# Performance work log

Hardware: AMD Instinct MI355X
Metric: run time of the kernel (lower is better)

## Reference

```python
import jax, jax.numpy as jnp
import numpy as np
import math

B, S, D, H = 2, 2048, 1024, 16
HD = D // H  # 64 head features


def setup_inputs() -> dict:
    key = jax.random.key(0)
    ks = jax.random.split(key, 6)
    x = jax.random.normal(ks[0], (B, S, D), jnp.float32)
    wq = jax.random.normal(ks[1], (D, D), jnp.float32) * 0.02
    wk = jax.random.normal(ks[2], (D, D), jnp.float32) * 0.02
    wv = jax.random.normal(ks[3], (D, D), jnp.float32) * 0.02
    wo = jax.random.normal(ks[4], (D, D), jnp.float32) * 0.02
    # Llama-style RoPE frequencies: unit-modulus complex per (pos, pair),
    # stored as separate cos/sin arrays of shape [S, HD//2].
    inv_freq = 1.0 / (10000.0 ** (jnp.arange(0, HD, 2, dtype=jnp.float32) / HD))
    ang = jnp.arange(S, dtype=jnp.float32)[:, None] * inv_freq[None, :]
    freq_cos = jnp.cos(ang)
    freq_sin = jnp.sin(ang)
    # realistic padding: each sequence keeps a random prefix of at least S//2 tokens
    lengths = jax.random.randint(ks[5], (B,), S // 2, S + 1)
    padding_mask = (jnp.arange(S)[None, :] < lengths[:, None]).astype(jnp.int32)
    return dict(x=x, wq=wq, wk=wk, wv=wv, wo=wo,
                freq_cos=freq_cos, freq_sin=freq_sin, padding_mask=padding_mask)


def _apply_rope(t, cos, sin):
    # t: [B, S, H, HD]; cos/sin: [S, HD//2]
    tr = t.reshape(t.shape[:-1] + (HD // 2, 2))
    t0, t1 = tr[..., 0], tr[..., 1]
    c = cos[None, :, None, :]
    s = sin[None, :, None, :]
    o0 = t0 * c - t1 * s  # real part of complex multiply
    o1 = t0 * s + t1 * c  # imag part
    return jnp.stack([o0, o1], axis=-1).reshape(t.shape)


def reference(x, wq, wk, wv, wo, freq_cos, freq_sin, padding_mask):
    # QKV projections (torch Linear: y = x @ W.T, no bias)
    q = (x @ wq.T).reshape(B, S, H, HD)
    k = (x @ wk.T).reshape(B, S, H, HD)
    v = (x @ wv.T).reshape(B, S, H, HD)
    q = _apply_rope(q, freq_cos, freq_sin)
    k = _apply_rope(k, freq_cos, freq_sin)
    q = jnp.transpose(q, (0, 2, 1, 3))  # [B,H,S,HD]
    k = jnp.transpose(k, (0, 2, 1, 3))
    v = jnp.transpose(v, (0, 2, 1, 3))
    # NOTE: original scales by sqrt(n_features), not sqrt(head_dim)
    scores = jnp.einsum('bhqd,bhkd->bhqk', q, k) / math.sqrt(D)
    bias = jnp.where(padding_mask[:, None, None, :] == 0,
                     jnp.float32(-jnp.inf), jnp.float32(0.0))
    p = jax.nn.softmax(scores + bias, axis=-1)
    out = jnp.einsum('bhqk,bhkd->bhqd', p, v)
    out = jnp.transpose(out, (0, 2, 1, 3)).reshape(B, S, D)
    return out @ wo.T
```

## Files before the change

### kernel.cpp

```cpp
#include <hip/hip_runtime.h>
#include <hip/hip_bf16.h>
#include <stdint.h>

typedef unsigned short u16;
typedef __attribute__((ext_vector_type(8))) short bf16x8;
typedef __attribute__((ext_vector_type(4))) float f32x4;
typedef __attribute__((ext_vector_type(16))) float f32x16;

__device__ __forceinline__ u16 f2bf(float f) {
  union { float f; uint32_t u; } a; a.f = f;
  return (u16)((a.u + 0x7FFFu + ((a.u >> 16) & 1u)) >> 16);
}

__device__ __forceinline__ void gload_lds16(const void* g, void* l) {
  auto* gp = (__attribute__((address_space(1))) void*)(uintptr_t)g;
  auto* lp = (__attribute__((address_space(3))) void*)(uintptr_t)l;
  __builtin_amdgcn_global_load_lds(gp, lp, 16, 0, 0);
}

__device__ __forceinline__ float exp2_fast(float x) {
  float r;
  asm("v_exp_f32 %0, %1" : "=v"(r) : "v"(x));
  return r;
}

#define CVTPK(d, a, b) asm("v_cvt_pk_bf16_f32 %0, %1, %2" : "=v"(d) : "v"(a), "v"(b))
#define SWAP32(a, b)   asm("v_permlane32_swap_b32 %0, %1" : "+v"(a), "+v"(b))
#define BARRIER() do { asm volatile("" ::: "memory"); __builtin_amdgcn_s_barrier(); asm volatile("" ::: "memory"); } while (0)
#define WAITVM0() asm volatile("s_waitcnt vmcnt(0)" ::: "memory")

__global__ void cvt_kernel(const float4* __restrict__ x, const float4* __restrict__ wq,
                           const float4* __restrict__ wk, const float4* __restrict__ wv,
                           const float4* __restrict__ wo,
                           ushort4* __restrict__ xb, ushort4* __restrict__ wqkv,
                           ushort4* __restrict__ wob) {
  const int XN = (2 * 2048 * 1024) / 4;
  const int WN = (1024 * 1024) / 4;
  const int total = XN + 4 * WN;
  for (int i = blockIdx.x * 256 + threadIdx.x; i < total; i += gridDim.x * 256) {
    float4 v; ushort4* dst;
    if (i < XN) { v = x[i]; dst = xb + i; }
    else {
      int j = i - XN; int m = j >> 18; int o = j & (WN - 1);
      const float4* src = (m == 0) ? wq : (m == 1) ? wk : (m == 2) ? wv : wo;
      v = src[o];
      dst = (m < 3) ? (wqkv + j) : (wob + o);
    }
    ushort4 r; r.x = f2bf(v.x); r.y = f2bf(v.y); r.z = f2bf(v.z); r.w = f2bf(v.w);
    *dst = r;
  }
}

__global__ void len_kernel(const int* __restrict__ mask, int* __restrict__ lens) {
  __shared__ int red[256];
  int b = blockIdx.x, s = 0;
  for (int i = threadIdx.x; i < 2048; i += 256) s += mask[b * 2048 + i];
  red[threadIdx.x] = s;
  __syncthreads();
  if (threadIdx.x < 64) {
    int v = red[threadIdx.x] + red[threadIdx.x + 64] + red[threadIdx.x + 128] + red[threadIdx.x + 192];
    #pragma unroll
    for (int o = 32; o > 0; o >>= 1) v += __shfl_down(v, o);
    if (threadIdx.x == 0) lens[b] = v;
  }
}

template <int BM, int BN, int MODE>
__global__ __launch_bounds__(256, 4)
void gemm2(const u16* __restrict__ A, const u16* __restrict__ Bm,
           int nTm, float* __restrict__ outf,
           u16* __restrict__ Qb, u16* __restrict__ Kb, u16* __restrict__ VbT,
           const float* __restrict__ cosT, const float* __restrict__ sinT) {
  constexpr int MREP = BM / 32;
  constexpr int NREP = BN / 32;
  constexpr int LA = BM / 64;
  constexpr int LB = BN / 64;
  __shared__ alignas(16) u16 SA[2][BM * 32];
  __shared__ alignas(16) u16 SB[2][BN * 32];

  const int tid = threadIdx.x, lane = tid & 63, wid = tid >> 6;
  const int wm = (wid >> 1) * (BM / 2), wn = (wid & 1) * (BN / 2);
  const int lr = lane & 15, lg = lane >> 4;

  const int cpx = gridDim.x >> 3;
  const int bid = (blockIdx.x & 7) * cpx + (blockIdx.x >> 3);
  const int m0 = (bid % nTm) * BM;
  const int n0 = (bid / nTm) * BN;

  const int srow = tid >> 2;
  const int schunk = (tid & 3) ^ (srow & 3);
  const u16* gA = A + (int64_t)(m0 + srow) * 1024 + schunk * 8;
  const u16* gB = Bm + (int64_t)(n0 + srow) * 1024 + schunk * 8;
  const int sdst = wid * 512;

#define STAGE(t) do { const int _b = (t) & 1, _ko = (t) * 32; \
    _Pragma("unroll") for (int j = 0; j < LA; ++j) \
      gload_lds16(gA + (int64_t)(j * 64) * 1024 + _ko, &SA[_b][j * 2048 + sdst]); \
    _Pragma("unroll") for (int j = 0; j < LB; ++j) \
      gload_lds16(gB + (int64_t)(j * 64) * 1024 + _ko, &SB[_b][j * 2048 + sdst]); } while (0)

  f32x4 acc[MREP][NREP];
  #pragma unroll
  for (int i = 0; i < MREP; ++i)
    #pragma unroll
    for (int j = 0; j < NREP; ++j)
      #pragma unroll
      for (int e = 0; e < 4; ++e) acc[i][j][e] = 0.0f;

  const int rchunk = (lg ^ (lr & 3)) * 8;

  STAGE(0);
  WAITVM0();
  BARRIER();

  for (int t = 0; t < 32; ++t) {
    if (t < 31) STAGE(t + 1);
    const u16* sa = SA[t & 1];
    const u16* sb = SB[t & 1];
    bf16x8 af[MREP], bfm[NREP];
    #pragma unroll
    for (int i = 0; i < MREP; ++i) af[i] = *(const bf16x8*)&sa[(wm + i * 16 + lr) * 32 + rchunk];
    #pragma unroll
    for (int i = 0; i < NREP; ++i) bfm[i] = *(const bf16x8*)&sb[(wn + i * 16 + lr) * 32 + rchunk];
    __builtin_amdgcn_s_setprio(1);
    #pragma unroll
    for (int mi = 0; mi < MREP; ++mi)
      #pragma unroll
      for (int ni = 0; ni < NREP; ++ni)
        acc[mi][ni] = __builtin_amdgcn_mfma_f32_16x16x32_bf16(af[mi], bfm[ni], acc[mi][ni], 0, 0, 0);
    __builtin_amdgcn_s_setprio(0);
    WAITVM0();
    BARRIER();
  }

  if (MODE == 0) {
    #pragma unroll
    for (int mi = 0; mi < MREP; ++mi)
      #pragma unroll
      for (int r = 0; r < 4; ++r) {
        const int row = m0 + wm + mi * 16 + lg * 4 + r;
        float* orow = outf + (int64_t)row * 1024 + n0 + wn + lr;
        #pragma unroll
        for (int ni = 0; ni < NREP; ++ni) orow[ni * 16] = acc[mi][ni][r];
      }
  } else {
    #pragma unroll
    for (int mi = 0; mi < MREP; ++mi) {
      #pragma unroll
      for (int r = 0; r < 4; ++r) {
        const int row = m0 + wm + mi * 16 + lg * 4 + r;
        const int bb = row >> 11, ss = row & 2047;
        #pragma unroll
        for (int ni = 0; ni < NREP; ++ni) {
          const int n = n0 + wn + ni * 16 + lr;
          float v = acc[mi][ni][r];
          if (n < 2048) {
            float partner = __shfl_xor(v, 1);
            const int ii = (n >> 1) & 31;
            const float c = cosT[ss * 32 + ii];
            const float sn = sinT[ss * 32 + ii];
            float rv = (n & 1) ? (partner * sn + v * c) : (v * c - partner * sn);
            const int h = (n >> 6) & 15, d = n & 63;
            const int idx = ((bb * 16 + h) * 2048 + ss) * 64 + d;
            if (n < 1024) Qb[idx] = f2bf(rv * 0.0450842298f);
            else          Kb[idx] = f2bf(rv);
          } else {
            const int n2 = n - 2048;
            const int h = n2 >> 6, d = n2 & 63;
            VbT[((int64_t)(bb * 16 + h) * 64 + d) * 2048 + ss] = f2bf(v);
          }
        }
      }
    }
  }
#undef STAGE
}

__global__ __launch_bounds__(256, 2)
void attn_kernel(const u16* __restrict__ Qb, const u16* __restrict__ Kb,
                 const u16* __restrict__ VbT, u16* __restrict__ attnb,
                 const int* __restrict__ lens) {
  __shared__ alignas(16) u16 Klds[2][64 * 64];
  __shared__ alignas(16) u16 Vlds[2][64 * 64];
  const int tid = threadIdx.x, lane = tid & 63, wid = tid >> 6;
  const int hi = lane >> 5, ql = lane & 31;
  const int bh = blockIdx.x >> 4;
  const int len = lens[bh >> 4];
  const int qrow = (blockIdx.x & 15) * 128 + wid * 32 + ql;

  bf16x8 qf[4];
  const u16* qptr = Qb + ((int64_t)bh * 2048 + qrow) * 64 + hi * 8;
  #pragma unroll
  for (int c = 0; c < 4; ++c) qf[c] = *(const bf16x8*)(qptr + c * 16);

  const int srow = tid >> 3, schunk = (tid & 7) ^ (srow & 7);
  const u16* kg = Kb + ((int64_t)bh * 2048 + srow) * 64 + schunk * 8;
  const u16* vg = VbT + ((int64_t)bh * 64 + srow) * 2048 + schunk * 8;
  const int dstoff = wid * 512;

  f32x16 oacc[2];
  #pragma unroll
  for (int r = 0; r < 16; ++r) { oacc[0][r] = 0.0f; oacc[1][r] = 0.0f; }
  float mrun = -1e30f, lrun = 0.0f;

  const int nt = (len + 63) >> 6;
  gload_lds16(kg,             &Klds[0][dstoff]);
  gload_lds16(kg + 32 * 64,   &Klds[0][2048 + dstoff]);
  gload_lds16(vg,             &Vlds[0][dstoff]);
  gload_lds16(vg + 32 * 2048, &Vlds[0][2048 + dstoff]);
  __syncthreads();

  const u16* kgn = kg + 64 * 64;
  const u16* vgn = vg + 64;

  for (int t = 0; t < nt; ++t) {
    const int bu = t & 1;
    if (t + 1 < nt) {
      gload_lds16(kgn,             &Klds[bu ^ 1][dstoff]);
      gload_lds16(kgn + 32 * 64,   &Klds[bu ^ 1][2048 + dstoff]);
      gload_lds16(vgn,             &Vlds[bu ^ 1][dstoff]);
      gload_lds16(vgn + 32 * 2048, &Vlds[bu ^ 1][2048 + dstoff]);
    }
    kgn += 64 * 64; vgn += 64;

    f32x16 s0, s1;
    #pragma unroll
    for (int r = 0; r < 16; ++r) { s0[r] = 0.0f; s1[r] = 0.0f; }
    __builtin_amdgcn_s_setprio(1);
    #pragma unroll
    for (int c = 0; c < 4; ++c) {
      const int slot = (((2 * c + hi) ^ (ql & 7)) * 8);
      bf16x8 kf0 = *(const bf16x8*)&Klds[bu][ql * 64 + slot];
      bf16x8 kf1 = *(const bf16x8*)&Klds[bu][(32 + ql) * 64 + slot];
      s0 = __builtin_amdgcn_mfma_f32_32x32x16_bf16(kf0, qf[c], s0, 0, 0, 0);
      s1 = __builtin_amdgcn_mfma_f32_32x32x16_bf16(kf1, qf[c], s1, 0, 0, 0);
    }
    __builtin_amdgcn_s_setprio(0);

    const int k0 = t * 64;
    if (k0 + 64 > len) {
      #pragma unroll
      for (int r = 0; r < 16; ++r) {
        const int key = k0 + (r & 3) + 8 * (r >> 2) + 4 * hi;
        if (key >= len) s0[r] = -1e30f;
        if (key + 32 >= len) s1[r] = -1e30f;
      }
    }

    float ma = fmaxf(s0[0], s1[0]), mb = fmaxf(s0[1], s1[1]);
    float mc = fmaxf(s0[2], s1[2]), md = fmaxf(s0[3], s1[3]);
    #pragma unroll
    for (int r = 4; r < 16; r += 4) {
      ma = fmaxf(ma, fmaxf(s0[r], s1[r]));
      mb = fmaxf(mb, fmaxf(s0[r + 1], s1[r + 1]));
      mc = fmaxf(mc, fmaxf(s0[r + 2], s1[r + 2]));
      md = fmaxf(md, fmaxf(s0[r + 3], s1[r + 3]));
    }
    float mx = fmaxf(fmaxf(ma, mb), fmaxf(mc, md));
    mx = fmaxf(mx, __shfl_xor(mx, 32));
    if (!__all(mx - mrun <= 11.0f)) {
      const float mnew = fmaxf(mrun, mx);
      const float sc = exp2_fast(mrun - mnew);
      #pragma unroll
      for (int r = 0; r < 16; ++r) { oacc[0][r] *= sc; oacc[1][r] *= sc; }
      lrun *= sc;
      mrun = mnew;
    }
    float p[32];
    float ps0 = 0.0f, ps1 = 0.0f, ps2 = 0.0f, ps3 = 0.0f;
    #pragma unroll
    for (int r = 0; r < 16; r += 4) {
      p[r]      = exp2_fast(s0[r] - mrun);
      p[r + 1]  = exp2_fast(s0[r + 1] - mrun);
      p[r + 2]  = exp2_fast(s0[r + 2] - mrun);
      p[r + 3]  = exp2_fast(s0[r + 3] - mrun);
      p[16 + r]     = exp2_fast(s1[r] - mrun);
      p[16 + r + 1] = exp2_fast(s1[r + 1] - mrun);
      p[16 + r + 2] = exp2_fast(s1[r + 2] - mrun);
      p[16 + r + 3] = exp2_fast(s1[r + 3] - mrun);
      ps0 += p[r] + p[16 + r];
      ps1 += p[r + 1] + p[16 + r + 1];
      ps2 += p[r + 2] + p[16 + r + 2];
      ps3 += p[r + 3] + p[16 + r + 3];
    }
    float psum = (ps0 + ps1) + (ps2 + ps3);
    psum += __shfl_xor(psum, 32);
    lrun += psum;

    bf16x8 pfrag[4];
    #pragma unroll
    for (int ks = 0; ks < 4; ++ks) {
      uint32_t a0, a1, a2, a3;
      CVTPK(a0, p[8 * ks + 0], p[8 * ks + 1]);
      CVTPK(a1, p[8 * ks + 2], p[8 * ks + 3]);
      CVTPK(a2, p[8 * ks + 4], p[8 * ks + 5]);
      CVTPK(a3, p[8 * ks + 6], p[8 * ks + 7]);
      SWAP32(a0, a2);
      SWAP32(a1, a3);
      union { uint32_t u[4]; bf16x8 v; } pw;
      pw.u[0] = a0; pw.u[1] = a1; pw.u[2] = a2; pw.u[3] = a3;
      pfrag[ks] = pw.v;
    }

    __builtin_amdgcn_s_setprio(1);
    #pragma unroll
    for (int dc = 0; dc < 2; ++dc) {
      const int drow = dc * 32 + ql;
      #pragma unroll
      for (int ks = 0; ks < 4; ++ks) {
        const int slot = (((2 * ks + hi) ^ (ql & 7)) * 8);
        bf16x8 vf = *(const bf16x8*)&Vlds[bu][drow * 64 + slot];
        oacc[dc] = __builtin_amdgcn_mfma_f32_32x32x16_bf16(vf, pfrag[ks], oacc[dc], 0, 0, 0);
      }
    }
    __builtin_amdgcn_s_setprio(0);
    __syncthreads();
  }

  const float inv = 1.0f / lrun;
  u16* outp = attnb + ((int64_t)((bh >> 4) * 2048 + qrow)) * 1024 + (bh & 15) * 64;
  #pragma unroll
  for (int dc = 0; dc < 2; ++dc)
    #pragma unroll
    for (int g = 0; g < 4; ++g) {
      ushort4 w;
      w.x = f2bf(oacc[dc][4 * g + 0] * inv);
      w.y = f2bf(oacc[dc][4 * g + 1] * inv);
      w.z = f2bf(oacc[dc][4 * g + 2] * inv);
      w.w = f2bf(oacc[dc][4 * g + 3] * inv);
      *(ushort4*)(outp + dc * 32 + 8 * g + 4 * hi) = w;
    }
}

extern "C" void kernel_launch(void* const* d_in, const int* in_sizes, int n_in,
                              void* d_out, int out_size, void* d_ws, size_t ws_size,
                              hipStream_t stream) {
  const float* x    = (const float*)d_in[0];
  const float* wq   = (const float*)d_in[1];
  const float* wk   = (const float*)d_in[2];
  const float* wv   = (const float*)d_in[3];
  const float* wo   = (const float*)d_in[4];
  const float* fcos = (const float*)d_in[5];
  const float* fsin = (const float*)d_in[6];
  const int*   pmsk = (const int*)d_in[7];
  float* out = (float*)d_out;

  char* ws = (char*)d_ws;
  u16* XB    = (u16*)(ws);
  u16* WQKV  = (u16*)(ws + (size_t)8  * 1048576);
  u16* WOB   = (u16*)(ws + (size_t)14 * 1048576);
  u16* QB    = (u16*)(ws + (size_t)16 * 1048576);
  u16* KB    = (u16*)(ws + (size_t)24 * 1048576);
  u16* VBT   = (u16*)(ws + (size_t)32 * 1048576);
  u16* ATTNB = (u16*)(ws + (size_t)40 * 1048576);
  int* LENS  = (int*)(ws + (size_t)48 * 1048576);

  cvt_kernel<<<2048, 256, 0, stream>>>((const float4*)x, (const float4*)wq,
                                       (const float4*)wk, (const float4*)wv,
                                       (const float4*)wo, (ushort4*)XB,
                                       (ushort4*)WQKV, (ushort4*)WOB);
  len_kernel<<<2, 256, 0, stream>>>(pmsk, LENS);

  gemm2<128, 128, 1><<<768, 256, 0, stream>>>(XB, WQKV, 32, nullptr,
                                              QB, KB, VBT, fcos, fsin);

  attn_kernel<<<512, 256, 0, stream>>>(QB, KB, VBT, ATTNB, LENS);

  gemm2<128, 64, 0><<<512, 256, 0, stream>>>(ATTNB, WOB, 32, out,
                                             nullptr, nullptr, nullptr, nullptr, nullptr);
}
```

Before: 124.5 us.

## Triple-buffer GEMM LDS stages with partial vmcnt waits and new swizzle

Measured after the change: 121.5 us. 2.4% less time.

```diff
diff --git a/kernel.cpp b/kernel.cpp
--- a/kernel.cpp
+++ b/kernel.cpp
@@ -24,10 +24,15 @@
   return r;
 }
 
+template <int N> __device__ __forceinline__ void waitvm() {
+  if constexpr (N == 3)      asm volatile("s_waitcnt vmcnt(3)" ::: "memory");
+  else if constexpr (N == 4) asm volatile("s_waitcnt vmcnt(4)" ::: "memory");
+  else                       asm volatile("s_waitcnt vmcnt(0)" ::: "memory");
+}
+
 #define CVTPK(d, a, b) asm("v_cvt_pk_bf16_f32 %0, %1, %2" : "=v"(d) : "v"(a), "v"(b))
 #define SWAP32(a, b)   asm("v_permlane32_swap_b32 %0, %1" : "+v"(a), "+v"(b))
 #define BARRIER() do { asm volatile("" ::: "memory"); __builtin_amdgcn_s_barrier(); asm volatile("" ::: "memory"); } while (0)
-#define WAITVM0() asm volatile("s_waitcnt vmcnt(0)" ::: "memory")
 
 __global__ void cvt_kernel(const float4* __restrict__ x, const float4* __restrict__ wq,
                            const float4* __restrict__ wk, const float4* __restrict__ wv,
@@ -66,8 +71,8 @@
 }
 
 template <int BM, int BN, int MODE>
-__global__ __launch_bounds__(256, 4)
-void gemm2(const u16* __restrict__ A, const u16* __restrict__ Bm,
+__global__ __launch_bounds__(256, 3)
+void gemm3(const u16* __restrict__ A, const u16* __restrict__ Bm,
            int nTm, float* __restrict__ outf,
            u16* __restrict__ Qb, u16* __restrict__ Kb, u16* __restrict__ VbT,
            const float* __restrict__ cosT, const float* __restrict__ sinT) {
@@ -75,8 +80,9 @@
   constexpr int NREP = BN / 32;
   constexpr int LA = BM / 64;
   constexpr int LB = BN / 64;
-  __shared__ alignas(16) u16 SA[2][BM * 32];
-  __shared__ alignas(16) u16 SB[2][BN * 32];
+  constexpr int LOADS = LA + LB;
+  __shared__ alignas(16) u16 SA[3][BM * 32];
+  __shared__ alignas(16) u16 SB[3][BN * 32];
 
   const int tid = threadIdx.x, lane = tid & 63, wid = tid >> 6;
   const int wm = (wid >> 1) * (BM / 2), wn = (wid & 1) * (BN / 2);
@@ -88,16 +94,16 @@
   const int n0 = (bid / nTm) * BN;
 
   const int srow = tid >> 2;
-  const int schunk = (tid & 3) ^ (srow & 3);
+  const int schunk = (tid & 3) ^ ((srow >> 1) & 3);
   const u16* gA = A + (int64_t)(m0 + srow) * 1024 + schunk * 8;
   const u16* gB = Bm + (int64_t)(n0 + srow) * 1024 + schunk * 8;
   const int sdst = wid * 512;
 
-#define STAGE(t) do { const int _b = (t) & 1, _ko = (t) * 32; \
+#define STAGE(b, t) do { const int _ko = (t) * 32; \
     _Pragma("unroll") for (int j = 0; j < LA; ++j) \
-      gload_lds16(gA + (int64_t)(j * 64) * 1024 + _ko, &SA[_b][j * 2048 + sdst]); \
+      gload_lds16(gA + (int64_t)(j * 64) * 1024 + _ko, &SA[b][j * 2048 + sdst]); \
     _Pragma("unroll") for (int j = 0; j < LB; ++j) \
-      gload_lds16(gB + (int64_t)(j * 64) * 1024 + _ko, &SB[_b][j * 2048 + sdst]); } while (0)
+      gload_lds16(gB + (int64_t)(j * 64) * 1024 + _ko, &SB[b][j * 2048 + sdst]); } while (0)
 
   f32x4 acc[MREP][NREP];
   #pragma unroll
@@ -107,30 +113,33 @@
       #pragma unroll
       for (int e = 0; e < 4; ++e) acc[i][j][e] = 0.0f;
 
-  const int rchunk = (lg ^ (lr & 3)) * 8;
-
-  STAGE(0);
-  WAITVM0();
+  const int rchunk = (lg ^ ((lr >> 1) & 3)) * 8;
+
+  STAGE(0, 0);
+  STAGE(1, 1);
+  waitvm<LOADS>();
   BARRIER();
 
+  int bc = 0, bs = 2;
   for (int t = 0; t < 32; ++t) {
-    if (t < 31) STAGE(t + 1);
-    const u16* sa = SA[t & 1];
-    const u16* sb = SB[t & 1];
+    if (t < 30) STAGE(bs, t + 2);
+    const u16* sa = SA[bc];
+    const u16* sb = SB[bc];
     bf16x8 af[MREP], bfm[NREP];
     #pragma unroll
     for (int i = 0; i < MREP; ++i) af[i] = *(const bf16x8*)&sa[(wm + i * 16 + lr) * 32 + rchunk];
     #pragma unroll
     for (int i = 0; i < NREP; ++i) bfm[i] = *(const bf16x8*)&sb[(wn + i * 16 + lr) * 32 + rchunk];
-    __builtin_amdgcn_s_setprio(1);
     #pragma unroll
     for (int mi = 0; mi < MREP; ++mi)
       #pragma unroll
       for (int ni = 0; ni < NREP; ++ni)
         acc[mi][ni] = __builtin_amdgcn_mfma_f32_16x16x32_bf16(af[mi], bfm[ni], acc[mi][ni], 0, 0, 0);
-    __builtin_amdgcn_s_setprio(0);
-    WAITVM0();
+    if (t < 30) waitvm<LOADS>();
+    else        waitvm<0>();
     BARRIER();
+    bc = (bc == 2) ? 0 : bc + 1;
+    bs = (bs == 2) ? 0 : bs + 1;
   }
 
   if (MODE == 0) {
@@ -361,11 +370,11 @@
                                        (ushort4*)WQKV, (ushort4*)WOB);
   len_kernel<<<2, 256, 0, stream>>>(pmsk, LENS);
 
-  gemm2<128, 128, 1><<<768, 256, 0, stream>>>(XB, WQKV, 32, nullptr,
+  gemm3<128, 128, 1><<<768, 256, 0, stream>>>(XB, WQKV, 32, nullptr,
                                               QB, KB, VBT, fcos, fsin);
 
   attn_kernel<<<512, 256, 0, stream>>>(QB, KB, VBT, ATTNB, LENS);
 
-  gemm2<128, 64, 0><<<512, 256, 0, stream>>>(ATTNB, WOB, 32, out,
+  gemm3<128, 64, 0><<<512, 256, 0, stream>>>(ATTNB, WOB, 32, out,
                                              nullptr, nullptr, nullptr, nullptr, nullptr);
 }
```
